# Optimization experiments

Hardware: AMD Instinct MI355X
Metric: run time of the kernel (lower is better)

The kernel has to match this reference:

```python
import jax, jax.numpy as jnp
import numpy as np
from jax import lax
from jax.scipy.special import gammaln

B, T_FEATS, T_TEXT = 16, 2000, 400
ADIM, ODIM = 256, 512
BIG_NEG = -1e30
BLANK_LOGP = -1.0  # log(blank_prob) with blank_prob = e**-1


def _conv1d(x, w, b, pad):
    # x: (B, C_in, L), w: (C_out, C_in, K)
    y = lax.conv_general_dilated(x, w, (1,), [(pad, pad)],
                                 dimension_numbers=('NCH', 'OIH', 'NCH'))
    return y + b[None, :, None]


def _betabinom_prior(T, N):
    # ESPnet AlignmentModule beta-binomial attention prior (w=1):
    # alpha_t = t (1..T), beta_t = T - t + 1, k = 1..N, n = N
    t = jnp.arange(1, T + 1, dtype=jnp.float32)
    a = t[:, None]                                   # (T,1)
    bb = (T - t + 1.0)[:, None]                      # (T,1)
    k = jnp.arange(1, N + 1, dtype=jnp.float32)[None, :]  # (1,N)
    n = float(N)
    betaln = lambda x, y: gammaln(x) + gammaln(y) - gammaln(x + y)
    logC = gammaln(n + 1.0) - gammaln(k + 1.0) - gammaln(n - k + 1.0)
    return logC + betaln(k + a, n - k + bb) - betaln(a, bb)  # (T,N)


def _alignment_encoder(txt, speech, tw1, tb1, tw2, tb2, fw1, fb1, fw2, fb2, fw3, fb3):
    t = txt.transpose(0, 2, 1)                       # (B, adim, T_text)
    t = jax.nn.relu(_conv1d(t, tw1, tb1, 1))
    t = _conv1d(t, tw2, tb2, 0)
    t = t.transpose(0, 2, 1)                         # (B, T_text, adim)

    f = speech.transpose(0, 2, 1)                    # (B, odim, T_feats)
    f = jax.nn.relu(_conv1d(f, fw1, fb1, 1))
    f = jax.nn.relu(_conv1d(f, fw2, fb2, 1))
    f = _conv1d(f, fw3, fb3, 0)
    f = f.transpose(0, 2, 1)                         # (B, T_feats, adim)

    # score = -||f_t - t_s||_2 via expansion (avoids (B,T,S,D) intermediate)
    d2 = (jnp.sum(f * f, -1)[:, :, None] + jnp.sum(t * t, -1)[:, None, :]
          - 2.0 * jnp.einsum('btd,bsd->bts', f, t))
    score = -jnp.sqrt(jnp.maximum(d2, 1e-12))        # (B, T_feats, T_text)
    logp = jax.nn.log_softmax(score, axis=-1)
    return logp + _betabinom_prior(T_FEATS, T_TEXT)[None]


def _forwardsum_loss(log_p_attn):
    # CTC forward algorithm; targets are 1..N (all distinct) + interleaved blanks
    Bv, T, N = log_p_attn.shape
    lp = jnp.concatenate(
        [jnp.full((Bv, T, 1), BLANK_LOGP, log_p_attn.dtype), log_p_attn], axis=-1)
    lp = jax.nn.log_softmax(lp, axis=-1)             # (B, T, N+1)
    S = 2 * N + 1
    ext = np.zeros(S, np.int32); ext[1::2] = np.arange(1, N + 1)
    skip_ok = np.zeros(S, bool); skip_ok[3::2] = True  # non-blank, distinct labels
    ext = jnp.asarray(ext); skip_ok = jnp.asarray(skip_ok)

    emit = lp[:, :, ext]                             # (B, T, S)
    alpha = jnp.full((Bv, S), BIG_NEG)
    alpha = alpha.at[:, 0].set(emit[:, 0, 0]).at[:, 1].set(emit[:, 0, 1])

    def step(alpha, e):
        a1 = jnp.concatenate([jnp.full((Bv, 1), BIG_NEG), alpha[:, :-1]], axis=1)
        a2 = jnp.concatenate([jnp.full((Bv, 2), BIG_NEG), alpha[:, :-2]], axis=1)
        a2 = jnp.where(skip_ok[None, :], a2, BIG_NEG)
        alpha = jnp.logaddexp(jnp.logaddexp(alpha, a1), a2) + e
        return alpha, None

    alpha, _ = lax.scan(step, alpha, jnp.moveaxis(emit[:, 1:], 1, 0))
    nll = -jnp.logaddexp(alpha[:, -1], alpha[:, -2])  # (B,)
    # F.ctc_loss reduction='mean' divides each sample's nll by target length
    return jnp.mean(nll / N)


def _mas_single(lp):
    # lp: (T_feats, T_text) -> monotonic alignment (T_feats,) int32
    log_prob = lp.T                                  # (N, T)
    N, T = T_TEXT, T_FEATS
    q0 = jnp.where(jnp.arange(N) == 0, log_prob[0, 0], BIG_NEG)

    def fwd(q, col):
        q = jnp.maximum(q, jnp.concatenate([jnp.full((1,), BIG_NEG), q[:-1]])) + col
        return q, q

    _, qs = lax.scan(fwd, q0, log_prob[:, 1:].T)     # (T-1, N)
    Q = lax.stop_gradient(jnp.concatenate([q0[None], qs], axis=0))  # (T, N)

    def bwd(a_next, q_col):
        i_a = jnp.maximum(a_next - 1, 0)
        a = jnp.where(a_next == 0, 0,
                      jnp.where(q_col[i_a] >= q_col[a_next], i_a, a_next))
        a = a.astype(jnp.int32)
        return a, a

    _, A_rev = lax.scan(bwd, jnp.array(N - 1, jnp.int32), Q[:-1], reverse=True)
    return jnp.concatenate([A_rev, jnp.array([N - 1], jnp.int32)])  # (T,)


def _viterbi_decode(log_p_attn):
    A = jax.vmap(_mas_single)(log_p_attn)            # (B, T_feats) int32
    ds = jax.vmap(lambda a: jnp.bincount(a, length=T_TEXT))(A)
    ds = ds.astype(log_p_attn.dtype)                 # (B, T_text) durations
    gathered = jnp.take_along_axis(log_p_attn, A[:, :, None], axis=2)[..., 0]
    bin_loss = -jnp.mean(jnp.mean(gathered, axis=1))
    return ds, bin_loss


def setup_inputs() -> dict:
    key = jax.random.key(0)
    ks = jax.random.split(key, 12)
    s = 0.05
    inp = {
        'speech': jax.random.normal(ks[0], (B, T_FEATS, ODIM), jnp.float32),
        'txt': jax.random.normal(ks[1], (B, T_TEXT, ADIM), jnp.float32),
        'speech_len': jnp.full((B,), T_FEATS, jnp.int32),
        'txt_len': jnp.full((B,), T_TEXT, jnp.int32),
        'tw1': jax.random.normal(ks[2], (ADIM, ADIM, 3)) * s,
        'tb1': jnp.zeros((ADIM,)),
        'tw2': jax.random.normal(ks[3], (ADIM, ADIM, 1)) * s,
        'tb2': jnp.zeros((ADIM,)),
        'fw1': jax.random.normal(ks[4], (ADIM, ODIM, 3)) * s,
        'fb1': jnp.zeros((ADIM,)),
        'fw2': jax.random.normal(ks[5], (ADIM, ADIM, 3)) * s,
        'fb2': jnp.zeros((ADIM,)),
        'fw3': jax.random.normal(ks[6], (ADIM, ADIM, 1)) * s,
        'fb3': jnp.zeros((ADIM,)),
    }
    return inp


def reference(speech, txt, speech_len, txt_len,
              tw1, tb1, tw2, tb2, fw1, fb1, fw2, fb2, fw3, fb3):
    # lengths are full (no padding), so masks are no-ops
    log_p_attn = _alignment_encoder(txt, speech, tw1, tb1, tw2, tb2,
                                    fw1, fb1, fw2, fb2, fw3, fb3)
    forwardsum_loss = _forwardsum_loss(log_p_attn)
    ds, bin_loss = _viterbi_decode(log_p_attn)
    return ds, bin_loss, forwardsum_loss, log_p_attn
```

## Files before the change

### kernel.cpp

```cpp
#include <hip/hip_runtime.h>
#include <math.h>

typedef unsigned int u32;
typedef unsigned long long u64;
typedef unsigned short u16;
typedef __attribute__((ext_vector_type(8))) _Float16 f16x8;
typedef __attribute__((ext_vector_type(4))) float f32x4;

#define BIGN (-1e30f)

static constexpr int NB = 16;
static constexpr int TF = 2000;
static constexpr int TT = 400;

__device__ __forceinline__ float wsum(float v){
#pragma unroll
  for(int o=32;o;o>>=1) v += __shfl_xor(v,o,64);
  return v;
}
__device__ __forceinline__ float EXP2(float x){ return __builtin_amdgcn_exp2f(x); }
__device__ __forceinline__ float LOG2(float x){ return __builtin_amdgcn_logf(x); }
__device__ __forceinline__ float lse2b(float x, float y){
  float m = fmaxf(x,y);
  return m + LOG2(1.0f + EXP2(-fabsf(x-y)));
}
__device__ __forceinline__ float lse3b(float x, float y, float z){
  float mx = fmaxf(fmaxf(x,y),z);
  float md = __builtin_amdgcn_fmed3f(x,y,z);
  float mn = fminf(fminf(x,y),z);
  return mx + LOG2(1.0f + EXP2(md-mx) + EXP2(mn-mx));
}
__device__ __forceinline__ u16 f2h(float v){
  _Float16 h = (_Float16)v;
  return *(u16*)&h;
}
__device__ __forceinline__ float shup1(float v){
  int r = __builtin_amdgcn_update_dpp(__float_as_int(BIGN), __float_as_int(v),
                                      0x138, 0xf, 0xf, false);
  return __int_as_float(r);
}

__global__ void k_lgt(double* lgt){
  int m = blockIdx.x*blockDim.x + threadIdx.x;
  if(m < 2432) lgt[m] = (m>=1)? lgamma((double)m) : 0.0;
}
__global__ void k_terms(const double* __restrict__ lgt, double* rowA, double* colA, double* sA){
  int i = blockIdx.x*blockDim.x + threadIdx.x;
  if(i < TF)   rowA[i] = -lgt[2401] - lgt[i+1] - lgt[2000-i] + lgt[2001];
  if(i < TT)   colA[i] =  lgt[401]  - lgt[i+2] - lgt[400-i];
  if(i < 2399) sA[i]   =  lgt[i+2]  + lgt[2399-i];
}

__device__ __forceinline__ void packf(const float* __restrict__ w, u16* __restrict__ dst,
    int CIN, int KW, int i){
  int k = i % KW;
  int c = (i / KW) % CIN;
  int o = i / (KW*CIN);
  dst[((size_t)k*256 + o)*CIN + c] = f2h(w[i]);
}
__device__ __forceinline__ void cvtp(const float* __restrict__ src, u16* __restrict__ dst,
    int P, int C, int i){
  int c = i % C;
  int p = (i / C) % (P+2);
  int b = i / (C*(P+2));
  float v = 0.f;
  if(p>=1 && p<=P) v = src[((size_t)b*P + (p-1))*C + c];
  dst[i] = f2h(v);
}
__device__ __forceinline__ void zpr(u16* __restrict__ buf, int P, int j){
  int c = j % 256;
  int s = (j / 256) & 1;
  int b = j / 512;
  buf[((size_t)b*(P+2) + (s? P+1 : 0))*256 + c] = 0;
}
__global__ __launch_bounds__(256) void prep1_k(
    const float* __restrict__ fw1, const float* __restrict__ fw2, const float* __restrict__ fw3,
    const float* __restrict__ tw1, const float* __restrict__ tw2, const float* __restrict__ txt,
    u16* fw1p, u16* fw2p, u16* fw3p, u16* tw1p, u16* tw2p,
    u16* inbfT, u16* tout1, u16* out1){
  constexpr int N = 393216+196608+65536+196608+65536+1646592+8192+8192;
  for(int i = blockIdx.x*256 + threadIdx.x; i < N; i += gridDim.x*256){
    int j = i;
    if(j < 393216){ packf(fw1, fw1p, 512, 3, j); continue; } j -= 393216;
    if(j < 196608){ packf(fw2, fw2p, 256, 3, j); continue; } j -= 196608;
    if(j < 65536) { packf(fw3, fw3p, 256, 1, j); continue; } j -= 65536;
    if(j < 196608){ packf(tw1, tw1p, 256, 3, j); continue; } j -= 196608;
    if(j < 65536) { packf(tw2, tw2p, 256, 1, j); continue; } j -= 65536;
    if(j < 1646592){ cvtp(txt, inbfT, TT, 256, j); continue; } j -= 1646592;
    if(j < 8192) { zpr(tout1, TT, j); continue; } j -= 8192;
    zpr(out1, TF, j);
  }
}

__global__ __launch_bounds__(256) void cvt_pad_k(const float* __restrict__ src, u16* __restrict__ dst,
    int P, int C){
  int n = NB*(P+2)*C;
  for(int i = blockIdx.x*256 + threadIdx.x; i < n; i += gridDim.x*256) cvtp(src, dst, P, C, i);
}
__global__ __launch_bounds__(256) void zpad_k(u16* __restrict__ buf, int P){
  int n = NB*2*256;
  for(int i = blockIdx.x*256 + threadIdx.x; i < n; i += gridDim.x*256) zpr(buf, P, i);
}

template<int CIN, int KW, bool RELU, bool OBF>
__global__ __launch_bounds__(256) void mfconv_k(const u16* __restrict__ inb,
    const u16* __restrict__ wp, const float* __restrict__ bias, void* __restrict__ outp, int P){
  __shared__ __align__(16) u16 Al[4*66*8];
  __shared__ __align__(16) u16 Bl[KW*4*256*8];
  const int b = blockIdx.y;
  const int m0 = blockIdx.x * 64;
  const int tid = threadIdx.x;
  const int lane = tid & 63, wv = tid >> 6;
  const int lo16 = lane & 15, hi = lane >> 4;
  constexpr int K1 = (KW==1)? 1 : 0;
  const u16* inB = inb + (size_t)b*(P+2)*CIN;
  f32x4 acc[4][4];
#pragma unroll
  for(int i=0;i<4;i++)
#pragma unroll
    for(int j=0;j<4;j++) acc[i][j] = (f32x4){0.f,0.f,0.f,0.f};

  for(int c0=0; c0<CIN; c0+=32){
    __syncthreads();
    for(int idx = tid; idx < 264; idx += 256){
      int r = idx >> 2, q = idx & 3;
      int rowp = m0 + r;
      f16x8 v = (f16x8){0,0,0,0,0,0,0,0};
      if(rowp <= P+1) v = *(const f16x8*)&inB[(size_t)rowp*CIN + c0 + q*8];
      *(f16x8*)&Al[(q*66 + r)*8] = v;
    }
#pragma unroll
    for(int k=0;k<KW;k++){
      const u16* wr = &wp[((size_t)(k*256) + tid)*CIN + c0];
      f16x8 w0 = *(const f16x8*)&wr[0];
      f16x8 w1 = *(const f16x8*)&wr[8];
      f16x8 w2 = *(const f16x8*)&wr[16];
      f16x8 w3 = *(const f16x8*)&wr[24];
      *(f16x8*)&Bl[((k*4+0)*256 + tid)*8] = w0;
      *(f16x8*)&Bl[((k*4+1)*256 + tid)*8] = w1;
      *(f16x8*)&Bl[((k*4+2)*256 + tid)*8] = w2;
      *(f16x8*)&Bl[((k*4+3)*256 + tid)*8] = w3;
    }
    __syncthreads();
#pragma unroll
    for(int k=0;k<KW;k++){
      f16x8 af[4];
#pragma unroll
      for(int rf=0;rf<4;rf++)
        af[rf] = *(const f16x8*)&Al[(hi*66 + rf*16 + lo16 + k + K1)*8];
#pragma unroll
      for(int cf=0;cf<4;cf++){
        int o = wv*64 + cf*16 + lo16;
        f16x8 bf = *(const f16x8*)&Bl[((k*4+hi)*256 + o)*8];
#pragma unroll
        for(int rf=0;rf<4;rf++)
          acc[rf][cf] = __builtin_amdgcn_mfma_f32_16x16x32_f16(af[rf], bf, acc[rf][cf], 0, 0, 0);
      }
    }
  }
#pragma unroll
  for(int cf=0;cf<4;cf++){
    int o = wv*64 + cf*16 + lo16;
    float bs = bias[o];
#pragma unroll
    for(int rf=0;rf<4;rf++){
#pragma unroll
      for(int j=0;j<4;j++){
        int p = m0 + rf*16 + hi*4 + j;
        if(p < P){
          float v = acc[rf][cf][j] + bs;
          if(RELU) v = fmaxf(v, 0.f);
          if(OBF) ((u16*)outp)[((size_t)b*(P+2) + p + 1)*256 + o] = f2h(v);
          else    ((float*)outp)[((size_t)b*P + p)*256 + o] = v;
        }
      }
    }
  }
}

__global__ __launch_bounds__(256) void norm2b_k(const float* __restrict__ x1, const float* __restrict__ x2,
    float* __restrict__ o1, float* __restrict__ o2){
  int r = blockIdx.x*4 + (threadIdx.x>>6);
  int lane = threadIdx.x & 63;
  const float* src; float* dst; int rr;
  if(r < NB*TF){ src = x1; dst = o1; rr = r; }
  else { rr = r - NB*TF; if(rr >= NB*TT) return; src = x2; dst = o2; }
  float4 v = ((const float4*)(src + (size_t)rr*256))[lane];
  float s = v.x*v.x + v.y*v.y + v.z*v.z + v.w*v.w;
  s = wsum(s);
  if(lane==0) dst[rr] = s;
}

__global__ __launch_bounds__(256) void score_gemm(const float* __restrict__ F, const float* __restrict__ Tn,
    const float* __restrict__ fn2, const float* __restrict__ tn2, float* __restrict__ outp){
  constexpr int KC = 32;
  __shared__ __align__(16) float As[KC][68];
  __shared__ __align__(16) float Bs[KC][68];
  const int b = blockIdx.z;
  const int t0 = blockIdx.y*64, s0 = blockIdx.x*64;
  const int tid = threadIdx.x, tx = tid&15, ty = tid>>4;
  const float* Fb = F  + (size_t)b*TF*256;
  const float* Tb = Tn + (size_t)b*TT*256;
  float acc[4][4] = {};
  const int lk = tid & 31, lt0 = (tid>>5)*8;
  for(int k0=0;k0<256;k0+=KC){
    __syncthreads();
#pragma unroll
    for(int i=0;i<8;i++){
      int t = t0 + lt0 + i;
      As[lk][lt0+i] = (t<TF)? Fb[(size_t)t*256 + k0 + lk] : 0.f;
      int s = s0 + lt0 + i;
      Bs[lk][lt0+i] = (s<TT)? Tb[(size_t)s*256 + k0 + lk] : 0.f;
    }
    __syncthreads();
#pragma unroll
    for(int k=0;k<KC;k++){
      float a0[4], b0[4];
      *(float4*)a0 = *(const float4*)&As[k][ty*4];
      *(float4*)b0 = *(const float4*)&Bs[k][tx*4];
#pragma unroll
      for(int i=0;i<4;i++)
#pragma unroll
        for(int j=0;j<4;j++) acc[i][j] = fmaf(a0[i], b0[j], acc[i][j]);
    }
  }
#pragma unroll
  for(int i=0;i<4;i++){
    int t = t0 + ty*4 + i;
    if(t<TF){
      float fn = fn2[b*TF + t];
#pragma unroll
      for(int j=0;j<4;j++){
        int s = s0 + tx*4 + j;
        if(s<TT){
          float d2 = fn + tn2[b*TT + s] - 2.f*acc[i][j];
          outp[((size_t)b*TF + t)*TT + s] = -sqrtf(fmaxf(d2, 1e-12f));
        }
      }
    }
  }
}

__global__ __launch_bounds__(128) void softmax_prior_k(float* __restrict__ logp,
    const double* __restrict__ rowA, const double* __restrict__ colA, const double* __restrict__ sA,
    float* __restrict__ Z2){
  const int row = blockIdx.x;
  const int t0 = row % TF;
  float* rp = logp + (size_t)row*TT;
  const int tid = threadIdx.x;
  __shared__ float sh2[2];
  float v[4]; int ix[4];
#pragma unroll
  for(int i=0;i<4;i++){ ix[i] = tid + i*128; v[i] = (ix[i]<TT)? rp[ix[i]] : BIGN; }
  float m = fmaxf(fmaxf(v[0],v[1]),fmaxf(v[2],v[3]));
#pragma unroll
  for(int o=32;o;o>>=1) m = fmaxf(m, __shfl_xor(m,o,64));
  if((tid&63)==0) sh2[tid>>6] = m;
  __syncthreads();
  m = fmaxf(sh2[0], sh2[1]);
  float s = 0.f;
#pragma unroll
  for(int i=0;i<4;i++) if(ix[i]<TT) s += __expf(v[i]-m);
  s = wsum(s);
  __syncthreads();
  if((tid&63)==0) sh2[tid>>6] = s;
  __syncthreads();
  s = sh2[0] + sh2[1];
  const float lse = m + __logf(s);
  const double rA = rowA[t0];
  float f[4]; float m2 = BIGN;
#pragma unroll
  for(int i=0;i<4;i++){
    if(ix[i]<TT){
      float pr = (float)(colA[ix[i]] + sA[t0+ix[i]] + rA);
      f[i] = (v[i]-lse) + pr;
      rp[ix[i]] = f[i];
      m2 = fmaxf(m2, f[i]);
    } else f[i] = BIGN;
  }
#pragma unroll
  for(int o=32;o;o>>=1) m2 = fmaxf(m2, __shfl_xor(m2,o,64));
  __syncthreads();
  if((tid&63)==0) sh2[tid>>6] = m2;
  __syncthreads();
  m2 = fmaxf(fmaxf(sh2[0],sh2[1]), -1.0f);
  float s2 = (tid==0)? __expf(-1.0f - m2) : 0.f;
#pragma unroll
  for(int i=0;i<4;i++) if(ix[i]<TT) s2 += __expf(f[i]-m2);
  s2 = wsum(s2);
  __syncthreads();
  if((tid&63)==0) sh2[tid>>6] = s2;
  __syncthreads();
  if(tid==0) Z2[row] = m2 + __logf(sh2[0]+sh2[1]);
}

#define LCTC_STEP(E) { \
  float n1 = shup1(a[13]); \
  float w6 = lse2b(a[12], a[11]); \
  a[13] = lse2b(a[13], w6) + (E)[6];  a[12] = w6 + EBL; \
  float w5 = lse2b(a[10], a[9]); \
  a[11] = lse2b(a[11], w5) + (E)[5];  a[10] = w5 + EBL; \
  float w4 = lse2b(a[8], a[7]); \
  a[9]  = lse2b(a[9],  w4) + (E)[4];  a[8]  = w4 + EBL; \
  float w3 = lse2b(a[6], a[5]); \
  a[7]  = lse2b(a[7],  w3) + (E)[3];  a[6]  = w3 + EBL; \
  float w2 = lse2b(a[4], a[3]); \
  a[5]  = lse2b(a[5],  w2) + (E)[2];  a[4]  = w2 + EBL; \
  float w1 = lse2b(a[2], a[1]); \
  a[3]  = lse2b(a[3],  w1) + (E)[1];  a[2]  = w1 + EBL; \
  float w0 = lse2b(a[0], n1); \
  a[1]  = lse2b(a[1],  w0) + (E)[0];  a[0]  = w0 + EBL; }

#define CPREF(E, K) { int kk=(K); if(kk>999) kk=999; int row = dir? (TF-1-kk) : kk; \
  const float* rpp = lp + (size_t)row*TT; \
  (E)[0]=rpp[jc[0]]*IL2; (E)[1]=rpp[jc[1]]*IL2; (E)[2]=rpp[jc[2]]*IL2; (E)[3]=rpp[jc[3]]*IL2; \
  (E)[4]=rpp[jc[4]]*IL2; (E)[5]=rpp[jc[5]]*IL2; (E)[6]=rpp[jc[6]]*IL2; }

#define MAS_STEP(E, TIDX) { \
  float n1 = shup1(q[6]); \
  u32 byte = 0; \
  if(lane>0 && n1 >= q[0]) byte |= 1u; \
  if(q[0] >= q[1]) byte |= 2u; \
  if(q[1] >= q[2]) byte |= 4u; \
  if(q[2] >= q[3]) byte |= 8u; \
  if(q[3] >= q[4]) byte |= 16u; \
  if(q[4] >= q[5]) byte |= 32u; \
  if(q[5] >= q[6]) byte |= 64u; \
  cb[(size_t)((TIDX)-1)*64 + lane] = (unsigned char)byte; \
  q[6] = fmaxf(q[6], q[5]) + (E)[6]; \
  q[5] = fmaxf(q[5], q[4]) + (E)[5]; \
  q[4] = fmaxf(q[4], q[3]) + (E)[4]; \
  q[3] = fmaxf(q[3], q[2]) + (E)[3]; \
  q[2] = fmaxf(q[2], q[1]) + (E)[2]; \
  q[1] = fmaxf(q[1], q[0]) + (E)[1]; \
  q[0] = fmaxf(q[0], n1) + (E)[0]; }

#define MPREF(E, ROW) { int rr=(ROW); rr = (rr>TF-1)? (TF-1) : rr; const float* rpp = lp + (size_t)rr*TT; \
  (E)[0]=rpp[jc[0]]; (E)[1]=rpp[jc[1]]; (E)[2]=rpp[jc[2]]; (E)[3]=rpp[jc[3]]; \
  (E)[4]=rpp[jc[4]]; (E)[5]=rpp[jc[5]]; (E)[6]=rpp[jc[6]]; }

__global__ __launch_bounds__(128) __attribute__((amdgpu_waves_per_eu(1,1)))
void scan_k(const float* __restrict__ logp,
    const float* __restrict__ Z2, unsigned char* __restrict__ cmpb, float* __restrict__ nll){
  const int lane = threadIdx.x & 63;
  const int wave = threadIdx.x >> 6;
  constexpr float IL2 = 1.4426950408889634f;
  constexpr float L2  = 0.6931471805599453f;
  if(blockIdx.x < NB){
    const int b = blockIdx.x;
    const float* lp = logp + (size_t)b*TF*TT;
    __shared__ float af[801], ag[801];
    const int dir = wave;
    double zs = 0.0;
    if(wave==0){
      for(int t=lane; t<TF; t+=64) zs += (double)Z2[b*TF + t];
#pragma unroll
      for(int o=32;o;o>>=1) zs += __shfl_xor(zs, o, 64);
    }
    int jc[7];
#pragma unroll
    for(int i=0;i<7;i++){ int j = 7*lane + i; j = (j < TT)? j : (TT-1); jc[i] = dir? (TT-1-j) : j; }
    float a[14];
#pragma unroll
    for(int i=0;i<14;i++) a[i] = BIGN;
    if(lane==0){
      a[0] = -1.0f*IL2;
      a[1] = (dir? lp[(size_t)(TF-1)*TT + (TT-1)] : lp[0]) * IL2;
    }
    const float EBL = -1.0f*IL2;
    float e0[7],e1[7],e2[7],e3[7],e4[7],e5[7],e6[7],e7[7];
    CPREF(e0,1); CPREF(e1,2); CPREF(e2,3); CPREF(e3,4);
    CPREF(e4,5); CPREF(e5,6); CPREF(e6,7); CPREF(e7,8);
    int k = 1;
    for(; k + 8 <= 993; k += 8){
      LCTC_STEP(e0); CPREF(e0, k+8);
      LCTC_STEP(e1); CPREF(e1, k+9);
      LCTC_STEP(e2); CPREF(e2, k+10);
      LCTC_STEP(e3); CPREF(e3, k+11);
      LCTC_STEP(e4); CPREF(e4, k+12);
      LCTC_STEP(e5); CPREF(e5, k+13);
      LCTC_STEP(e6); CPREF(e6, k+14);
      LCTC_STEP(e7); CPREF(e7, k+15);
    }
    for(; k<=999; k++){
      float P[7];
      CPREF(P, k);
      LCTC_STEP(P);
    }
    float* dst = wave? ag : af;
#pragma unroll
    for(int i=0;i<14;i++){ int s = 14*lane+i; if(s<=800) dst[s] = a[i]; }
    __syncthreads();
    if(wave==0){
      float acc = BIGN;
#pragma unroll
      for(int i=0;i<14;i++){
        int s = 14*lane+i;
        if(s<=800){
          float x0 = af[s];
          float x1 = (s>=1)? af[s-1] : BIGN;
          float x2 = ((s&1) && s>=3)? af[s-2] : BIGN;
          float A1 = lse3b(x0,x1,x2);
          acc = lse2b(acc, A1 + ag[800-s]);
        }
      }
#pragma unroll
      for(int o=32;o;o>>=1) acc = lse2b(acc, __shfl_xor(acc,o,64));
      if(lane==0) nll[b] = -((acc*L2) - (float)zs);
    }
  } else {
    if(wave) return;
    const int b = blockIdx.x - NB;
    const float* lp = logp + (size_t)b*TF*TT;
    unsigned char* cb = cmpb + (size_t)b*TF*64;
    int jc[7];
#pragma unroll
    for(int i=0;i<7;i++){ int j = 7*lane + i; jc[i] = (j < TT)? j : (TT-1); }
    float q[7];
#pragma unroll
    for(int i=0;i<7;i++) q[i] = BIGN;
    if(lane==0) q[0] = lp[0];
    float e0[7],e1[7],e2[7],e3[7];
    MPREF(e0,1); MPREF(e1,2); MPREF(e2,3); MPREF(e3,4);
    int t0 = 1;
    for(; t0 + 4 <= TF; t0 += 4){
      MAS_STEP(e0, t0);   MPREF(e0, t0+4);
      MAS_STEP(e1, t0+1); MPREF(e1, t0+5);
      MAS_STEP(e2, t0+2); MPREF(e2, t0+6);
      MAS_STEP(e3, t0+3); MPREF(e3, t0+7);
    }
    for(; t0<TF; t0++){
      float P[7];
      MPREF(P, t0);
      MAS_STEP(P, t0);
    }
    {
      float n1 = shup1(q[6]);
      u32 byte = 0;
      if(lane>0 && n1 >= q[0]) byte |= 1u;
      if(q[0] >= q[1]) byte |= 2u;
      if(q[1] >= q[2]) byte |= 4u;
      if(q[2] >= q[3]) byte |= 8u;
      if(q[3] >= q[4]) byte |= 16u;
      if(q[4] >= q[5]) byte |= 32u;
      if(q[5] >= q[6]) byte |= 64u;
      cb[(size_t)(TF-1)*64 + lane] = (unsigned char)byte;
    }
  }
}

__global__ __launch_bounds__(256) void masback_k(const unsigned char* __restrict__ cmpb,
    const float* __restrict__ logp, float* __restrict__ ds, float* __restrict__ gsum){
  const int b = blockIdx.x;
  const unsigned char* cb = cmpb + (size_t)b*TF*64;
  __shared__ unsigned char bits[500*64];
  __shared__ short Ash[TF];
  __shared__ int cnt[TT];
  __shared__ float ps[4];
  int a = TT-1;
  for(int ch=3; ch>=0; ch--){
    const int tlo = ch*500;
    __syncthreads();
    for(int i=threadIdx.x;i<8000;i+=256) ((u32*)bits)[i] = ((const u32*)(cb + (size_t)tlo*64))[i];
    __syncthreads();
    if(threadIdx.x==0){
      int thi = tlo + 499;
      if(ch==3){ Ash[TF-1] = (short)(TT-1); thi = TF-2; }
      for(int t=thi;t>=tlo;t--){
        if(a > 0){
          unsigned char w = bits[(t-tlo)*64 + a/7];
          a -= (int)((w >> (a%7)) & 1u);
        }
        Ash[t] = (short)a;
      }
    }
  }
  __syncthreads();
  for(int i=threadIdx.x;i<TT;i+=256) cnt[i]=0;
  __syncthreads();
  float part = 0.f;
  const float* lp = logp + (size_t)b*TF*TT;
  for(int t=threadIdx.x;t<TF;t+=256){
    int at = Ash[t];
    atomicAdd(&cnt[at], 1);
    part += lp[(size_t)t*TT + at];
  }
  __syncthreads();
  for(int i=threadIdx.x;i<TT;i+=256) ds[(size_t)b*TT + i] = (float)cnt[i];
  part = wsum(part);
  if((threadIdx.x&63)==0) ps[threadIdx.x>>6] = part;
  __syncthreads();
  if(threadIdx.x==0) gsum[b] = ps[0]+ps[1]+ps[2]+ps[3];
}

__global__ void final_k(const float* __restrict__ nll, const float* __restrict__ gsum, float* __restrict__ out){
  if(threadIdx.x==0 && blockIdx.x==0){
    float fs=0.f, bs=0.f;
    for(int b=0;b<NB;b++){ fs += nll[b] / (float)TT; bs += gsum[b] / (float)TF; }
    out[6400] = -(bs / (float)NB);
    out[6401] = fs / (float)NB;
  }
}

extern "C" void kernel_launch(void* const* d_in, const int* in_sizes, int n_in,
                              void* d_out, int out_size, void* d_ws, size_t ws_size,
                              hipStream_t stream){
  const float* speech = (const float*)d_in[0];
  const float* txt    = (const float*)d_in[1];
  const float* tw1 = (const float*)d_in[4];
  const float* tb1 = (const float*)d_in[5];
  const float* tw2 = (const float*)d_in[6];
  const float* tb2 = (const float*)d_in[7];
  const float* fw1 = (const float*)d_in[8];
  const float* fb1 = (const float*)d_in[9];
  const float* fw2 = (const float*)d_in[10];
  const float* fb2 = (const float*)d_in[11];
  const float* fw3 = (const float*)d_in[12];
  const float* fb3 = (const float*)d_in[13];
  float* out  = (float*)d_out;
  float* ds   = out;
  float* logp = out + 6402;
  char* ws = (char*)d_ws;
  double* lgt  = (double*)(ws + 0);
  double* rowA = (double*)(ws + 20480);
  double* colA = (double*)(ws + 36864);
  double* sA   = (double*)(ws + 40960);
  float*  nll  = (float*)(ws + 61440);
  float*  gsum = (float*)(ws + 61696);
  float*  Z2   = (float*)(ws + 65536);
  float*  fn2  = (float*)(ws + 196608);
  float*  tn2  = (float*)(ws + 327680);
  unsigned char* cmpb = (unsigned char*)(ws + 360448);
  float*  tenc = (float*)(ws + 2408448);
  float*  f1   = (float*)(ws + 8962048);
  if(ws_size < 41730048) return;

  char* lr = (char*)(((uintptr_t)logp + 255) & ~(uintptr_t)255);
  u16* inbfT = (u16*)lr;
  u16* tout1 = (u16*)(lr + 4000000);
  u16* inbfA = (u16*)lr;
  u16* out2  = (u16*)lr;
  u16* wbase = (u16*)(lr + 32900000);
  u16* fw1p = wbase;
  u16* fw2p = wbase + 393216;
  u16* fw3p = wbase + 589824;
  u16* tw1p = wbase + 655360;
  u16* tw2p = wbase + 851968;
  u16* out1  = (u16*)(lr + 34750000);

  k_lgt  <<<10,256,0,stream>>>(lgt);
  k_terms<<<10,256,0,stream>>>(lgt,rowA,colA,sA);

  prep1_k<<<2048,256,0,stream>>>(fw1,fw2,fw3,tw1,tw2, txt,
                                 fw1p,fw2p,fw3p,tw1p,tw2p, inbfT, tout1, out1);

  mfconv_k<256,3,true ,true ><<<dim3(7,NB),256,0,stream>>>(inbfT, tw1p, tb1, tout1, TT);
  mfconv_k<256,1,false,false><<<dim3(7,NB),256,0,stream>>>(tout1, tw2p, tb2, tenc, TT);

  cvt_pad_k<<<4096,256,0,stream>>>(speech, inbfA, TF, 512);
  mfconv_k<512,3,true ,true ><<<dim3(32,NB),256,0,stream>>>(inbfA, fw1p, fb1, out1, TF);
  zpad_k<<<32,256,0,stream>>>(out2, TF);
  mfconv_k<256,3,true ,true ><<<dim3(32,NB),256,0,stream>>>(out1, fw2p, fb2, out2, TF);
  mfconv_k<256,1,false,false><<<dim3(32,NB),256,0,stream>>>(out2, fw3p, fb3, f1, TF);

  norm2b_k<<<(NB*TF+NB*TT)/4,256,0,stream>>>(f1, tenc, fn2, tn2);

  score_gemm<<<dim3(7,32,NB),256,0,stream>>>(f1, tenc, fn2, tn2, logp);
  softmax_prior_k<<<NB*TF,128,0,stream>>>(logp, rowA, colA, sA, Z2);

  scan_k<<<2*NB,128,0,stream>>>(logp, Z2, cmpb, nll);
  masback_k<<<NB,256,0,stream>>>(cmpb, logp, ds, gsum);
  final_k<<<1,64,0,stream>>>(nll, gsum, out);
}
```

Measured before the change: 883.0 us.

## Split CTC forward/backward scan state across two waves per direction

The CTC alpha/beta scan previously held 14 states per lane in a single wave per direction. It now splits the 801 states across two waves per direction, 8 states per lane, and passes the boundary value between them through shared memory with a __syncthreads every time step. This shortens the serial dependency chain per step and cuts register pressure. The cost is about 1000 block-wide barriers, and the MAS blocks now launch with 256 threads, so extra idle waves are created and then exit.

```diff
diff --git a/kernel.cpp b/kernel.cpp
--- a/kernel.cpp
+++ b/kernel.cpp
@@ -294,27 +294,25 @@
   if(tid==0) Z2[row] = m2 + __logf(sh2[0]+sh2[1]);
 }
 
-#define LCTC_STEP(E) { \
-  float n1 = shup1(a[13]); \
-  float w6 = lse2b(a[12], a[11]); \
-  a[13] = lse2b(a[13], w6) + (E)[6];  a[12] = w6 + EBL; \
-  float w5 = lse2b(a[10], a[9]); \
-  a[11] = lse2b(a[11], w5) + (E)[5];  a[10] = w5 + EBL; \
-  float w4 = lse2b(a[8], a[7]); \
-  a[9]  = lse2b(a[9],  w4) + (E)[4];  a[8]  = w4 + EBL; \
+#define LCTC8(E, KV) { \
+  float bv = bnd[dir][((KV)-1)&1]; \
+  float n1 = shup1(a[7]); \
+  if(half && lane==0) n1 = bv; \
+  float w0 = lse2b(a[0], n1); \
+  float w1 = lse2b(a[2], a[1]); \
+  float w2 = lse2b(a[4], a[3]); \
   float w3 = lse2b(a[6], a[5]); \
-  a[7]  = lse2b(a[7],  w3) + (E)[3];  a[6]  = w3 + EBL; \
-  float w2 = lse2b(a[4], a[3]); \
-  a[5]  = lse2b(a[5],  w2) + (E)[2];  a[4]  = w2 + EBL; \
-  float w1 = lse2b(a[2], a[1]); \
-  a[3]  = lse2b(a[3],  w1) + (E)[1];  a[2]  = w1 + EBL; \
-  float w0 = lse2b(a[0], n1); \
-  a[1]  = lse2b(a[1],  w0) + (E)[0];  a[0]  = w0 + EBL; }
-
-#define CPREF(E, K) { int kk=(K); if(kk>999) kk=999; int row = dir? (TF-1-kk) : kk; \
+  a[7] = lse2b(a[7], w3) + (E)[3]; \
+  a[5] = lse2b(a[5], w2) + (E)[2]; \
+  a[3] = lse2b(a[3], w1) + (E)[1]; \
+  a[1] = lse2b(a[1], w0) + (E)[0]; \
+  a[6] = w3 + EBL; a[4] = w2 + EBL; a[2] = w1 + EBL; a[0] = w0 + EBL; \
+  if(half==0 && lane==52) bnd[dir][(KV)&1] = a[7]; \
+  __syncthreads(); }
+
+#define CPREF4(E, K) { int kk=(K); if(kk>999) kk=999; int row = dir? (TF-1-kk) : kk; \
   const float* rpp = lp + (size_t)row*TT; \
-  (E)[0]=rpp[jc[0]]*IL2; (E)[1]=rpp[jc[1]]*IL2; (E)[2]=rpp[jc[2]]*IL2; (E)[3]=rpp[jc[3]]*IL2; \
-  (E)[4]=rpp[jc[4]]*IL2; (E)[5]=rpp[jc[5]]*IL2; (E)[6]=rpp[jc[6]]*IL2; }
+  (E)[0]=rpp[jc[0]]*IL2; (E)[1]=rpp[jc[1]]*IL2; (E)[2]=rpp[jc[2]]*IL2; (E)[3]=rpp[jc[3]]*IL2; }
 
 #define MAS_STEP(E, TIDX) { \
   float n1 = shup1(q[6]); \
@@ -339,7 +337,7 @@
   (E)[0]=rpp[jc[0]]; (E)[1]=rpp[jc[1]]; (E)[2]=rpp[jc[2]]; (E)[3]=rpp[jc[3]]; \
   (E)[4]=rpp[jc[4]]; (E)[5]=rpp[jc[5]]; (E)[6]=rpp[jc[6]]; }
 
-__global__ __launch_bounds__(128) __attribute__((amdgpu_waves_per_eu(1,1)))
+__global__ __launch_bounds__(256) __attribute__((amdgpu_waves_per_eu(1,1)))
 void scan_k(const float* __restrict__ logp,
     const float* __restrict__ Z2, unsigned char* __restrict__ cmpb, float* __restrict__ nll){
   const int lane = threadIdx.x & 63;
@@ -350,59 +348,68 @@
     const int b = blockIdx.x;
     const float* lp = logp + (size_t)b*TF*TT;
     __shared__ float af[801], ag[801];
-    const int dir = wave;
+    __shared__ float bnd[2][2];
+    const int dir  = wave >> 1;
+    const int half = wave & 1;
+    const int base = half ? 424 : 0;
     double zs = 0.0;
     if(wave==0){
       for(int t=lane; t<TF; t+=64) zs += (double)Z2[b*TF + t];
 #pragma unroll
       for(int o=32;o;o>>=1) zs += __shfl_xor(zs, o, 64);
     }
-    int jc[7];
-#pragma unroll
-    for(int i=0;i<7;i++){ int j = 7*lane + i; j = (j < TT)? j : (TT-1); jc[i] = dir? (TT-1-j) : j; }
-    float a[14];
-#pragma unroll
-    for(int i=0;i<14;i++) a[i] = BIGN;
-    if(lane==0){
+    int jc[4];
+#pragma unroll
+    for(int i=0;i<4;i++){
+      int j = base/2 + 4*lane + i;
+      if(dir) j = TT-1-j;
+      jc[i] = (j < 0)? 0 : ((j > TT-1)? TT-1 : j);
+    }
+    float a[8];
+#pragma unroll
+    for(int i=0;i<8;i++) a[i] = BIGN;
+    if(half==0 && lane==0){
       a[0] = -1.0f*IL2;
       a[1] = (dir? lp[(size_t)(TF-1)*TT + (TT-1)] : lp[0]) * IL2;
     }
     const float EBL = -1.0f*IL2;
-    float e0[7],e1[7],e2[7],e3[7],e4[7],e5[7],e6[7],e7[7];
-    CPREF(e0,1); CPREF(e1,2); CPREF(e2,3); CPREF(e3,4);
-    CPREF(e4,5); CPREF(e5,6); CPREF(e6,7); CPREF(e7,8);
+    if(half==0 && lane==52) bnd[dir][0] = a[7];
+    float e0[4],e1[4],e2[4],e3[4],e4[4],e5[4],e6[4],e7[4];
+    CPREF4(e0,1); CPREF4(e1,2); CPREF4(e2,3); CPREF4(e3,4);
+    CPREF4(e4,5); CPREF4(e5,6); CPREF4(e6,7); CPREF4(e7,8);
+    __syncthreads();
     int k = 1;
     for(; k + 8 <= 993; k += 8){
-      LCTC_STEP(e0); CPREF(e0, k+8);
-      LCTC_STEP(e1); CPREF(e1, k+9);
-      LCTC_STEP(e2); CPREF(e2, k+10);
-      LCTC_STEP(e3); CPREF(e3, k+11);
-      LCTC_STEP(e4); CPREF(e4, k+12);
-      LCTC_STEP(e5); CPREF(e5, k+13);
-      LCTC_STEP(e6); CPREF(e6, k+14);
-      LCTC_STEP(e7); CPREF(e7, k+15);
+      LCTC8(e0, k);   CPREF4(e0, k+8);
+      LCTC8(e1, k+1); CPREF4(e1, k+9);
+      LCTC8(e2, k+2); CPREF4(e2, k+10);
+      LCTC8(e3, k+3); CPREF4(e3, k+11);
+      LCTC8(e4, k+4); CPREF4(e4, k+12);
+      LCTC8(e5, k+5); CPREF4(e5, k+13);
+      LCTC8(e6, k+6); CPREF4(e6, k+14);
+      LCTC8(e7, k+7); CPREF4(e7, k+15);
     }
     for(; k<=999; k++){
-      float P[7];
-      CPREF(P, k);
-      LCTC_STEP(P);
-    }
-    float* dst = wave? ag : af;
-#pragma unroll
-    for(int i=0;i<14;i++){ int s = 14*lane+i; if(s<=800) dst[s] = a[i]; }
+      float P[4];
+      CPREF4(P, k);
+      LCTC8(P, k);
+    }
+    float* dst = dir? ag : af;
+#pragma unroll
+    for(int i=0;i<8;i++){
+      int s = base + 8*lane + i;
+      if(half){ if(s<=800) dst[s] = a[i]; }
+      else    { if(s<=423) dst[s] = a[i]; }
+    }
     __syncthreads();
     if(wave==0){
       float acc = BIGN;
-#pragma unroll
-      for(int i=0;i<14;i++){
-        int s = 14*lane+i;
-        if(s<=800){
-          float x0 = af[s];
-          float x1 = (s>=1)? af[s-1] : BIGN;
-          float x2 = ((s&1) && s>=3)? af[s-2] : BIGN;
-          float A1 = lse3b(x0,x1,x2);
-          acc = lse2b(acc, A1 + ag[800-s]);
-        }
+      for(int s = lane; s <= 800; s += 64){
+        float x0 = af[s];
+        float x1 = (s>=1)? af[s-1] : BIGN;
+        float x2 = ((s&1) && s>=3)? af[s-2] : BIGN;
+        float A1 = lse3b(x0,x1,x2);
+        acc = lse2b(acc, A1 + ag[800-s]);
       }
 #pragma unroll
       for(int o=32;o;o>>=1) acc = lse2b(acc, __shfl_xor(acc,o,64));
@@ -568,7 +575,7 @@
   score_gemm<<<dim3(7,32,NB),256,0,stream>>>(f1, tenc, fn2, tn2, logp);
   softmax_prior_k<<<NB*TF,128,0,stream>>>(logp, rowA, colA, sA, Z2);
 
-  scan_k<<<2*NB,128,0,stream>>>(logp, Z2, cmpb, nll);
+  scan_k<<<2*NB,256,0,stream>>>(logp, Z2, cmpb, nll);
   masback_k<<<NB,256,0,stream>>>(cmpb, logp, ds, gsum);
   final_k<<<1,64,0,stream>>>(nll, gsum, out);
 }
```

Result: faster. 818.6 us (-7.3%).
